# Kernel tuning notes

Hardware: AMD Instinct MI355X
Metric: run time of the kernel (lower is better)

The kernel has to match this reference:

```python
import jax, jax.numpy as jnp
import numpy as np

WIN = 10
HEADS = 4


def _rel_index(win):
    ys, xs = jnp.meshgrid(jnp.arange(win), jnp.arange(win), indexing='ij')
    return xs - ys + win - 1


def _shift_mask(win_num, win):
    # last window gets -100 on cross-block (B, C) quadrants, 0 on diagonal blocks
    s = win // 2
    last = jnp.full((win, win), -100.0, dtype=jnp.float32)
    last = last.at[:s, :s].set(0.0)
    last = last.at[s:, s:].set(0.0)
    mask = jnp.zeros((win_num, win, win), dtype=jnp.float32)
    return mask.at[-1].set(last)


def setup_inputs() -> dict:
    key = jax.random.key(0)
    ks = jax.random.split(key, 6)
    B, WN, S, E = 16, 4096, WIN, 96
    return {
        'X': jax.random.normal(ks[0], (B, WN, S, E), dtype=jnp.float32),
        'W_qkv': jax.random.normal(ks[1], (E, 3 * E), dtype=jnp.float32) * 0.02,
        'b_qkv': jax.random.normal(ks[2], (3 * E,), dtype=jnp.float32) * 0.02,
        'W_o': jax.random.normal(ks[3], (E, E), dtype=jnp.float32) * 0.02,
        'b_o': jax.random.normal(ks[4], (E,), dtype=jnp.float32) * 0.02,
        'pos_bias': jax.random.normal(ks[5], (2 * WIN - 1, HEADS), dtype=jnp.float32) * 0.02,
    }


def reference(X, W_qkv, b_qkv, W_o, b_o, pos_bias):
    B, WN, S, E = X.shape
    H = HEADS
    dh = E // H
    scale = dh ** (-0.5)

    qkv = X @ W_qkv + b_qkv                       # (B, WN, S, 3E)
    qkv = qkv.reshape(B, WN, S, 3, H, dh).transpose(3, 0, 1, 4, 2, 5)  # (3,B,WN,H,S,dh)
    q, k, v = qkv[0], qkv[1], qkv[2]

    attn = jnp.einsum('bwhqd,bwhkd->bwhqk', q, k) * scale  # (B,WN,H,S,S)

    rel = pos_bias[_rel_index(S)]                 # (S, S, H)
    attn = attn + rel.transpose(2, 0, 1)[None, None]       # + (1,1,H,S,S)

    mask = _shift_mask(WN, S)                     # (WN, S, S)
    attn = attn + mask[None, :, None]             # broadcast over B, H

    proba = jax.nn.softmax(attn, axis=-1)
    out = jnp.einsum('bwhqk,bwhkd->bwhqd', proba, v)       # (B,WN,H,S,dh)
    out = out.transpose(0, 1, 3, 2, 4).reshape(B, WN, S, E)
    return out @ W_o + b_o
```

## Files before the change

kernel.cpp:

```cpp
#include <hip/hip_runtime.h>
#include <hip/hip_bf16.h>

typedef __attribute__((ext_vector_type(8))) short bf16x8;
typedef __attribute__((ext_vector_type(4))) float f32x4;
typedef __attribute__((ext_vector_type(4))) short short4v;

static __device__ __forceinline__ short f2bf(float f) {
    __hip_bfloat16 h = __float2bfloat16(f);
    short s; __builtin_memcpy(&s, &h, 2); return s;
}

#define WIN_TOT 65536
#define WN_MASK 4095
#define SEQ 10
#define EDIM 96
#define DHEAD 24
#define N3 288
#define G 8
#define ROWS 80
#define XPITCH 104
#define NGROUPS 8
#define WPB 64
#define NBLOCKS 1024
#define NTHREADS 512

#define XO_OFF    0
#define XO_BYTES  (ROWS*XPITCH*2)
#define Q_OFF     (XO_OFF + XO_BYTES)
#define QK_BYTES  (G*4*16*32*2)
#define K_OFF     (Q_OFF + QK_BYTES)
#define VT_OFF    (K_OFF + QK_BYTES)
#define VT_BYTES  (G*4*32*32*2)
#define P_OFF     (VT_OFF + VT_BYTES)
#define P_BYTES   (8*16*32*2)
#define POS_OFF   (P_OFF + P_BYTES)
#define POS_BYTES (320)
#define SMEM_BYTES (POS_OFF + POS_BYTES)

__global__ __launch_bounds__(NTHREADS, 1)
void swin_msa_fused(const float* __restrict__ X,
                    const float* __restrict__ Wqkv,
                    const float* __restrict__ bqkv,
                    const float* __restrict__ Wo,
                    const float* __restrict__ bo,
                    const float* __restrict__ pos,
                    float* __restrict__ out)
{
    extern __shared__ char smem[];
    short* xo = (short*)(smem + XO_OFF);
    short* qs = (short*)(smem + Q_OFF);
    short* ks = (short*)(smem + K_OFF);
    short* vt = (short*)(smem + VT_OFF);
    short* pb = (short*)(smem + P_OFF);
    float* posf = (float*)(smem + POS_OFF);

    const int tid  = threadIdx.x;
    const int wave = tid >> 6;
    const int lane = tid & 63;
    const int l15  = lane & 15;
    const int quad = lane >> 4;
    const int h    = wave & 3;
    const int k0   = quad * 8;

    {
        uint4* z = (uint4*)(smem + Q_OFF);
        const int n16 = (POS_OFF - Q_OFF) / 16;
        for (int i = tid; i < n16; i += NTHREADS) z[i] = make_uint4(0u,0u,0u,0u);
    }
    for (int i = tid; i < 76; i += NTHREADS) posf[i] = pos[i];

    bf16x8 bw[3][2][3];
    float biasqkv[3][2];
#pragma unroll
    for (int p = 0; p < 3; ++p)
#pragma unroll
      for (int t = 0; t < 2; ++t) {
        const int d = t*16 + l15;
        const bool valid = d < DHEAD;
        const int ncol = p*EDIM + h*DHEAD + (valid ? d : 0);
        biasqkv[p][t] = valid ? bqkv[ncol] : 0.f;
#pragma unroll
        for (int kk = 0; kk < 3; ++kk) {
          bf16x8 f;
#pragma unroll
          for (int jj = 0; jj < 8; ++jj) {
            const int krow = kk*32 + k0 + jj;
            f[jj] = valid ? f2bf(Wqkv[krow*N3 + ncol]) : (short)0;
          }
          bw[p][t][kk] = f;
        }
      }
    bf16x8 bwo[3];
    float bo_val = 0.f;
    if (wave < 6) {
      const int col = wave*16 + l15;
      bo_val = bo[col];
#pragma unroll
      for (int kk = 0; kk < 3; ++kk) {
        bf16x8 f;
#pragma unroll
        for (int jj = 0; jj < 8; ++jj) {
          const int krow = kk*32 + k0 + jj;
          f[jj] = f2bf(Wo[krow*EDIM + col]);
        }
        bwo[kk] = f;
      }
    }
    __syncthreads();

    const float scale = 0.20412414523193154f;
    const int wb0 = blockIdx.x * WPB;

    for (int g = 0; g < NGROUPS; ++g) {
      const int wbase = wb0 + g*G;
      const long rowbase = (long)wbase * SEQ;

      {
        const float4* src = (const float4*)(X + rowbase * (long)EDIM);
        for (int c = tid; c < ROWS*24; c += NTHREADS) {
          float4 v = src[c];
          const int r = c / 24, cc = c - r*24;
          short4v s4 = { f2bf(v.x), f2bf(v.y), f2bf(v.z), f2bf(v.w) };
          *(short4v*)&xo[r*XPITCH + cc*4] = s4;
        }
      }
      __syncthreads();

      for (int task = wave; task < 20; task += 8) {
        const int m = task >> 2;
        const bf16x8 a0 = *(const bf16x8*)&xo[(m*16 + l15)*XPITCH +  0 + k0];
        const bf16x8 a1 = *(const bf16x8*)&xo[(m*16 + l15)*XPITCH + 32 + k0];
        const bf16x8 a2 = *(const bf16x8*)&xo[(m*16 + l15)*XPITCH + 64 + k0];
#pragma unroll
        for (int p = 0; p < 3; ++p)
#pragma unroll
          for (int t = 0; t < 2; ++t) {
            f32x4 acc = {0.f,0.f,0.f,0.f};
            acc = __builtin_amdgcn_mfma_f32_16x16x32_bf16(a0, bw[p][t][0], acc, 0,0,0);
            acc = __builtin_amdgcn_mfma_f32_16x16x32_bf16(a1, bw[p][t][1], acc, 0,0,0);
            acc = __builtin_amdgcn_mfma_f32_16x16x32_bf16(a2, bw[p][t][2], acc, 0,0,0);
            const int d = t*16 + l15;
            if (d < DHEAD) {
              const float bias = biasqkv[p][t];
#pragma unroll
              for (int r = 0; r < 4; ++r) {
                const int R = m*16 + quad*4 + r;
                const int w = R / 10, s = R - w*10;
                float v = acc[r] + bias;
                if (p == 0) {
                  v *= scale;
                  qs[((w*4 + h)*16 + s)*32 + d] = f2bf(v);
                } else if (p == 1) {
                  ks[((w*4 + h)*16 + s)*32 + d] = f2bf(v);
                } else {
                  vt[((w*4 + h)*32 + d)*32 + s] = f2bf(v);
                }
              }
            }
          }
      }
      __syncthreads();

#pragma unroll
      for (int ii = 0; ii < 4; ++ii) {
        const int pair = wave*4 + ii;
        const int w = pair >> 2, hh = pair & 3;
        const short* qbase = qs + (w*4 + hh)*16*32;
        const short* kbase = ks + (w*4 + hh)*16*32;
        const bf16x8 qf = *(const bf16x8*)&qbase[l15*32 + k0];
        const bf16x8 kf = *(const bf16x8*)&kbase[l15*32 + k0];
        f32x4 sacc = {0.f,0.f,0.f,0.f};
        sacc = __builtin_amdgcn_mfma_f32_16x16x32_bf16(qf, kf, sacc, 0,0,0);
        const bool islast = ((wbase + w) & WN_MASK) == WN_MASK;
        const int j = l15;
        float pr[4];
#pragma unroll
        for (int r = 0; r < 4; ++r) {
          const int i = quad*4 + r;
          int idx = j - i + 9;
          idx = idx < 0 ? 0 : (idx > 18 ? 18 : idx);
          float sv = sacc[r] + posf[idx*4 + hh];
          if (islast && ((i < 5) != (j < 5))) sv -= 100.f;
          if (j >= 10) sv = -1e30f;
          float mx = sv;
          mx = fmaxf(mx, __shfl_xor(mx, 1, 16));
          mx = fmaxf(mx, __shfl_xor(mx, 2, 16));
          mx = fmaxf(mx, __shfl_xor(mx, 4, 16));
          mx = fmaxf(mx, __shfl_xor(mx, 8, 16));
          float e = __expf(sv - mx);
          float sm = e;
          sm += __shfl_xor(sm, 1, 16);
          sm += __shfl_xor(sm, 2, 16);
          sm += __shfl_xor(sm, 4, 16);
          sm += __shfl_xor(sm, 8, 16);
          pr[r] = e / sm;
        }
        short* pbw = pb + wave*16*32;
#pragma unroll
        for (int r = 0; r < 4; ++r)
          pbw[(quad*4 + r)*32 + j] = f2bf(pr[r]);
        asm volatile("" ::: "memory");
        const bf16x8 pf = *(const bf16x8*)&pbw[l15*32 + k0];
        asm volatile("" ::: "memory");
        const short* vbase = vt + (w*4 + hh)*32*32;
#pragma unroll
        for (int t = 0; t < 2; ++t) {
          const bf16x8 vf = *(const bf16x8*)&vbase[(t*16 + l15)*32 + k0];
          f32x4 oacc = {0.f,0.f,0.f,0.f};
          oacc = __builtin_amdgcn_mfma_f32_16x16x32_bf16(pf, vf, oacc, 0,0,0);
          const int d = t*16 + l15;
          if (d < DHEAD) {
#pragma unroll
            for (int r = 0; r < 4; ++r) {
              const int i = quad*4 + r;
              if (i < 10)
                xo[(w*10 + i)*XPITCH + hh*DHEAD + d] = f2bf(oacc[r]);
            }
          }
        }
      }
      __syncthreads();

      if (wave < 6) {
        for (int m = 0; m < 5; ++m) {
          const bf16x8 a0 = *(const bf16x8*)&xo[(m*16 + l15)*XPITCH +  0 + k0];
          const bf16x8 a1 = *(const bf16x8*)&xo[(m*16 + l15)*XPITCH + 32 + k0];
          const bf16x8 a2 = *(const bf16x8*)&xo[(m*16 + l15)*XPITCH + 64 + k0];
          f32x4 acc = {0.f,0.f,0.f,0.f};
          acc = __builtin_amdgcn_mfma_f32_16x16x32_bf16(a0, bwo[0], acc, 0,0,0);
          acc = __builtin_amdgcn_mfma_f32_16x16x32_bf16(a1, bwo[1], acc, 0,0,0);
          acc = __builtin_amdgcn_mfma_f32_16x16x32_bf16(a2, bwo[2], acc, 0,0,0);
          const int col = wave*16 + l15;
#pragma unroll
          for (int r = 0; r < 4; ++r) {
            const int R = m*16 + quad*4 + r;
            out[(rowbase + R)*EDIM + col] = acc[r] + bo_val;
          }
        }
      }
      __syncthreads();
    }
}

extern "C" void kernel_launch(void* const* d_in, const int* in_sizes, int n_in,
                              void* d_out, int out_size, void* d_ws, size_t ws_size,
                              hipStream_t stream) {
    const float* X    = (const float*)d_in[0];
    const float* Wqkv = (const float*)d_in[1];
    const float* bqkv = (const float*)d_in[2];
    const float* Wo   = (const float*)d_in[3];
    const float* bo   = (const float*)d_in[4];
    const float* pos  = (const float*)d_in[5];
    float* out = (float*)d_out;

    (void)hipFuncSetAttribute((const void*)swin_msa_fused,
                              hipFuncAttributeMaxDynamicSharedMemorySize,
                              SMEM_BYTES);
    swin_msa_fused<<<dim3(NBLOCKS), dim3(NTHREADS), SMEM_BYTES, stream>>>(
        X, Wqkv, bqkv, Wo, bo, pos, out);
}
```

Before: 689.1 us.

## Halve window group, raise occupancy, prefetch next X tile, pad LDS pitches

Each group now covers 4 windows instead of 8, and the grid doubles to 2048 blocks. Launch bounds ask for 4 blocks per CU instead of 1, so more waves can hide latency. Each group's X tile is loaded into registers one iteration ahead and converted to bf16 in LDS during the next iteration, overlapping global loads with compute. The Q, K, V^T and P buffers use a compact padded pitch of 40, shrinking LDS and reducing bank conflicts. In exchange, the MFMA tiles now read past the valid rows into neighbouring buffers, which relies on masking, and the tighter register budget risks spills of the cached weight fragments.

```diff
diff --git a/kernel.cpp b/kernel.cpp
--- a/kernel.cpp
+++ b/kernel.cpp
@@ -10,34 +10,36 @@
     short s; __builtin_memcpy(&s, &h, 2); return s;
 }
 
-#define WIN_TOT 65536
 #define WN_MASK 4095
 #define SEQ 10
 #define EDIM 96
 #define DHEAD 24
 #define N3 288
-#define G 8
-#define ROWS 80
+#define G 4
+#define ROWS 40
 #define XPITCH 104
+#define QKP 40
+#define VTP 40
+#define PP  40
 #define NGROUPS 8
-#define WPB 64
-#define NBLOCKS 1024
+#define WPB 32
+#define NBLOCKS 2048
 #define NTHREADS 512
 
 #define XO_OFF    0
 #define XO_BYTES  (ROWS*XPITCH*2)
 #define Q_OFF     (XO_OFF + XO_BYTES)
-#define QK_BYTES  (G*4*16*32*2)
-#define K_OFF     (Q_OFF + QK_BYTES)
-#define VT_OFF    (K_OFF + QK_BYTES)
-#define VT_BYTES  (G*4*32*32*2)
+#define Q_BYTES   (G*4*SEQ*QKP*2)
+#define K_OFF     (Q_OFF + Q_BYTES)
+#define VT_OFF    (K_OFF + Q_BYTES)
+#define VT_BYTES  (G*4*DHEAD*VTP*2)
 #define P_OFF     (VT_OFF + VT_BYTES)
-#define P_BYTES   (8*16*32*2)
+#define P_BYTES   (8*16*PP*2)
 #define POS_OFF   (P_OFF + P_BYTES)
 #define POS_BYTES (320)
 #define SMEM_BYTES (POS_OFF + POS_BYTES)
 
-__global__ __launch_bounds__(NTHREADS, 1)
+__global__ __launch_bounds__(NTHREADS, 4)
 void swin_msa_fused(const float* __restrict__ X,
                     const float* __restrict__ Wqkv,
                     const float* __restrict__ bqkv,
@@ -61,6 +63,14 @@
     const int quad = lane >> 4;
     const int h    = wave & 3;
     const int k0   = quad * 8;
+    const int wb0  = blockIdx.x * WPB;
+
+    float4 p0, p1;
+    {
+        const float4* src = (const float4*)(X + (long)wb0 * SEQ * EDIM);
+        p0 = src[tid];
+        if (tid < ROWS*24 - NTHREADS) p1 = src[NTHREADS + tid];
+    }
 
     {
         uint4* z = (uint4*)(smem + Q_OFF);
@@ -109,24 +119,29 @@
     __syncthreads();
 
     const float scale = 0.20412414523193154f;
-    const int wb0 = blockIdx.x * WPB;
-
     for (int g = 0; g < NGROUPS; ++g) {
       const int wbase = wb0 + g*G;
       const long rowbase = (long)wbase * SEQ;
 
       {
-        const float4* src = (const float4*)(X + rowbase * (long)EDIM);
-        for (int c = tid; c < ROWS*24; c += NTHREADS) {
-          float4 v = src[c];
-          const int r = c / 24, cc = c - r*24;
-          short4v s4 = { f2bf(v.x), f2bf(v.y), f2bf(v.z), f2bf(v.w) };
-          *(short4v*)&xo[r*XPITCH + cc*4] = s4;
-        }
-      }
-      __syncthreads();
-
-      for (int task = wave; task < 20; task += 8) {
+        const int r = tid / 24, cc = tid - r*24;
+        short4v s4 = { f2bf(p0.x), f2bf(p0.y), f2bf(p0.z), f2bf(p0.w) };
+        *(short4v*)&xo[r*XPITCH + cc*4] = s4;
+        if (tid < ROWS*24 - NTHREADS) {
+          const int c1 = NTHREADS + tid;
+          const int r1 = c1 / 24, cc1 = c1 - r1*24;
+          short4v t4 = { f2bf(p1.x), f2bf(p1.y), f2bf(p1.z), f2bf(p1.w) };
+          *(short4v*)&xo[r1*XPITCH + cc1*4] = t4;
+        }
+      }
+      if (g + 1 < NGROUPS) {
+        const float4* src = (const float4*)(X + (long)(wbase + G) * SEQ * EDIM);
+        p0 = src[tid];
+        if (tid < ROWS*24 - NTHREADS) p1 = src[NTHREADS + tid];
+      }
+      __syncthreads();
+
+      for (int task = wave; task < 12; task += 8) {
         const int m = task >> 2;
         const bf16x8 a0 = *(const bf16x8*)&xo[(m*16 + l15)*XPITCH +  0 + k0];
         const bf16x8 a1 = *(const bf16x8*)&xo[(m*16 + l15)*XPITCH + 32 + k0];
@@ -145,15 +160,17 @@
 #pragma unroll
               for (int r = 0; r < 4; ++r) {
                 const int R = m*16 + quad*4 + r;
-                const int w = R / 10, s = R - w*10;
-                float v = acc[r] + bias;
-                if (p == 0) {
-                  v *= scale;
-                  qs[((w*4 + h)*16 + s)*32 + d] = f2bf(v);
-                } else if (p == 1) {
-                  ks[((w*4 + h)*16 + s)*32 + d] = f2bf(v);
-                } else {
-                  vt[((w*4 + h)*32 + d)*32 + s] = f2bf(v);
+                if (R < ROWS) {
+                  const int w = R / 10, s = R - w*10;
+                  float v = acc[r] + bias;
+                  if (p == 0) {
+                    v *= scale;
+                    qs[((w*4 + h)*SEQ + s)*QKP + d] = f2bf(v);
+                  } else if (p == 1) {
+                    ks[((w*4 + h)*SEQ + s)*QKP + d] = f2bf(v);
+                  } else {
+                    vt[((w*4 + h)*DHEAD + d)*VTP + s] = f2bf(v);
+                  }
                 }
               }
             }
@@ -162,13 +179,13 @@
       __syncthreads();
 
 #pragma unroll
-      for (int ii = 0; ii < 4; ++ii) {
-        const int pair = wave*4 + ii;
+      for (int ii = 0; ii < 2; ++ii) {
+        const int pair = wave*2 + ii;
         const int w = pair >> 2, hh = pair & 3;
-        const short* qbase = qs + (w*4 + hh)*16*32;
-        const short* kbase = ks + (w*4 + hh)*16*32;
-        const bf16x8 qf = *(const bf16x8*)&qbase[l15*32 + k0];
-        const bf16x8 kf = *(const bf16x8*)&kbase[l15*32 + k0];
+        const short* qbase = qs + (w*4 + hh)*SEQ*QKP;
+        const short* kbase = ks + (w*4 + hh)*SEQ*QKP;
+        const bf16x8 qf = *(const bf16x8*)&qbase[l15*QKP + k0];
+        const bf16x8 kf = *(const bf16x8*)&kbase[l15*QKP + k0];
         f32x4 sacc = {0.f,0.f,0.f,0.f};
         sacc = __builtin_amdgcn_mfma_f32_16x16x32_bf16(qf, kf, sacc, 0,0,0);
         const bool islast = ((wbase + w) & WN_MASK) == WN_MASK;
@@ -195,17 +212,17 @@
           sm += __shfl_xor(sm, 8, 16);
           pr[r] = e / sm;
         }
-        short* pbw = pb + wave*16*32;
+        short* pbw = pb + wave*16*PP;
 #pragma unroll
         for (int r = 0; r < 4; ++r)
-          pbw[(quad*4 + r)*32 + j] = f2bf(pr[r]);
+          pbw[(quad*4 + r)*PP + j] = f2bf(pr[r]);
         asm volatile("" ::: "memory");
-        const bf16x8 pf = *(const bf16x8*)&pbw[l15*32 + k0];
+        const bf16x8 pf = *(const bf16x8*)&pbw[l15*PP + k0];
         asm volatile("" ::: "memory");
-        const short* vbase = vt + (w*4 + hh)*32*32;
+        const short* vbase = vt + (w*4 + hh)*DHEAD*VTP;
 #pragma unroll
         for (int t = 0; t < 2; ++t) {
-          const bf16x8 vf = *(const bf16x8*)&vbase[(t*16 + l15)*32 + k0];
+          const bf16x8 vf = *(const bf16x8*)&vbase[(t*16 + l15)*VTP + k0];
           f32x4 oacc = {0.f,0.f,0.f,0.f};
           oacc = __builtin_amdgcn_mfma_f32_16x16x32_bf16(pf, vf, oacc, 0,0,0);
           const int d = t*16 + l15;
@@ -222,7 +239,7 @@
       __syncthreads();
 
       if (wave < 6) {
-        for (int m = 0; m < 5; ++m) {
+        for (int m = 0; m < 3; ++m) {
           const bf16x8 a0 = *(const bf16x8*)&xo[(m*16 + l15)*XPITCH +  0 + k0];
           const bf16x8 a1 = *(const bf16x8*)&xo[(m*16 + l15)*XPITCH + 32 + k0];
           const bf16x8 a2 = *(const bf16x8*)&xo[(m*16 + l15)*XPITCH + 64 + k0];
@@ -234,7 +251,8 @@
 #pragma unroll
           for (int r = 0; r < 4; ++r) {
             const int R = m*16 + quad*4 + r;
-            out[(rowbase + R)*EDIM + col] = acc[r] + bo_val;
+            if (R < ROWS)
+              out[(rowbase + R)*EDIM + col] = acc[r] + bo_val;
           }
         }
       }
```

Measured after the change: 1.101 ms. +59.7%, slower.
